# Optimization experiments

Hardware: AMD Instinct MI355X
Metric: run time of the kernel (lower is better)

## Reference

```python
import jax, jax.numpy as jnp
import numpy as np

B = 512
NODES_PER_GRAPH = 256
N = B * NODES_PER_GRAPH
IN_DIM = 128
HID = 128
PAD_VALUE = -10000.0


def setup_inputs() -> dict:
    key = jax.random.key(0)
    ks = jax.random.split(key, 10)
    inp = {
        "last_node_batch": jax.random.normal(ks[0], (B, IN_DIM), jnp.float32),
        "h": jax.random.normal(ks[1], (N, HID), jnp.float32),
        # NodeEmbed: Linear(in_dim, hidden_dim)
        "W_embed": jax.random.normal(ks[2], (IN_DIM, HID), jnp.float32) / np.sqrt(IN_DIM),
        "b_embed": jnp.zeros((HID,), jnp.float32),
        # Linear_3(2H, 2H, 2)
        "W1": jax.random.normal(ks[3], (2 * HID, 2 * HID), jnp.float32) / np.sqrt(2 * HID),
        "b1": jnp.zeros((2 * HID,), jnp.float32),
        "W2": jax.random.normal(ks[4], (2 * HID, 2 * HID), jnp.float32) / np.sqrt(2 * HID),
        "b2": jnp.zeros((2 * HID,), jnp.float32),
        "W3": jax.random.normal(ks[5], (2 * HID, 2), jnp.float32) / np.sqrt(2 * HID),
        "b3": jnp.zeros((2,), jnp.float32),
        # ragged batch encoded as sorted segment ids (graph id per node)
        "segment_ids": jnp.repeat(jnp.arange(B, dtype=jnp.int64), NODES_PER_GRAPH),
        "max_nodes": NODES_PER_GRAPH,
    }
    return inp


def reference(last_node_batch, h, W_embed, b_embed, W1, b1, W2, b2, W3, b3,
              segment_ids, max_nodes):
    n = h.shape[0]
    b = last_node_batch.shape[0]
    # per-graph node embed, broadcast to each node of its graph (repeat+cat loop)
    node_embed = last_node_batch @ W_embed + b_embed          # [B, H]
    bcast = node_embed[segment_ids]                           # [N, H]
    stack = jnp.concatenate([h, bcast], axis=1)               # [N, 2H]
    # Linear_3 MLP
    out = jnp.tanh(stack @ W1 + b1)
    out = jnp.tanh(out @ W2 + b2)
    edges = out @ W3 + b3                                     # [N, 2]
    # unbatch + pad_sequence(padding_value=-10000), then flatten(1, -1)
    counts = jax.ops.segment_sum(jnp.ones((n,), jnp.int32), segment_ids, num_segments=b)
    offsets = jnp.cumsum(counts) - counts                     # start index of each graph
    pos = jnp.arange(n) - offsets[segment_ids]                # position within graph
    padded = jnp.full((b, max_nodes, 2), PAD_VALUE, dtype=edges.dtype)
    padded = padded.at[segment_ids, pos].set(edges)
    return padded.reshape(b, max_nodes * 2)
```

## Files before the change

kernel.cpp:

```cpp
#include <hip/hip_runtime.h>


typedef __attribute__((ext_vector_type(8))) short s16x8;
typedef __attribute__((ext_vector_type(4))) float f32x4;

#define K2   256
#define KH   128
#define LDK  264

__device__ __forceinline__ float b2f(unsigned short u) {
  return __builtin_bit_cast(float, (unsigned int)u << 16);
}
__device__ __forceinline__ unsigned short f2b(float f) {
  unsigned int u = __builtin_bit_cast(unsigned int, f);
  u += 0x7fffu + ((u >> 16) & 1u);
  return (unsigned short)(u >> 16);
}
__device__ __forceinline__ float fast_tanh(float x) {
  float ax = __builtin_fabsf(x);
  float t  = __builtin_amdgcn_exp2f(ax * -2.885390081777927f);
  float r  = (1.0f - t) * __builtin_amdgcn_rcpf(1.0f + t);
  return __builtin_copysignf(r, x);
}
__device__ __forceinline__ unsigned int probe_is16(const unsigned int* wraw,
                                                   int t) {
  unsigned int w = wraw[t];
  unsigned int e = (w >> 7) & 0xFFu;
  unsigned long long m = __ballot(e >= 96 && e < 128);
  return (__popcll(m) >= 32) ? 1u : 0u;
}

__global__ __launch_bounds__(256) void prep_pack(
    const void* __restrict__ W1, const void* __restrict__ W2,
    const void* __restrict__ Wemb,
    unsigned short* __restrict__ W1P, unsigned short* __restrict__ W2P)
{
  __shared__ unsigned int flagLds;
  const int blk = blockIdx.x, t = threadIdx.x;
  if (t < 64) { unsigned int f = probe_is16((const unsigned int*)Wemb, t);
                if (t == 0) flagLds = f; }
  __syncthreads();
  const bool is16 = flagLds != 0u;

  const void* S; unsigned short* D; int k0, n0, pk;
  if (blk < 32) { S = W1; D = W1P; pk = 2048;
                  k0 = (blk & 3) * 32; n0 = (blk >> 2) * 32; }
  else { int b = blk - 32; S = W2; D = W2P; pk = 4096;
         k0 = (b & 7) * 32; n0 = (b >> 3) * 32; }
  #pragma unroll
  for (int q = 0; q < 4; ++q) {
    int idx = t + 256 * q;
    int ln = idx & 31, lk = idx >> 5;
    int n = n0 + ln, k = k0 + lk;
    unsigned short v = is16 ? ((const unsigned short*)S)[k * K2 + n]
                            : f2b(((const float*)S)[k * K2 + n]);
    D[(n >> 4) * pk + (k >> 3) * 128 + (n & 15) * 8 + (k & 7)] = v;
  }
}

__global__ __launch_bounds__(512, 4) void mlp_fused(
    const void* __restrict__ h,     const void* __restrict__ last,
    const void* __restrict__ Wemb,  const void* __restrict__ bemb,
    const void* __restrict__ W1,    const void* __restrict__ b1,
    const void* __restrict__ b2,    const void* __restrict__ W3,
    const void* __restrict__ b3,
    const unsigned short* __restrict__ W1P,
    const unsigned short* __restrict__ W2P,
    void* __restrict__ out)
{
  __shared__ __align__(16) unsigned short smA[128 * LDK];
  __shared__ float embf[KH];
  __shared__ float ebias[K2];
  __shared__ float w3s[2 * K2];
  __shared__ float b3s[2];
  __shared__ float headp[128 * 8];
  __shared__ unsigned int flagLds;

  const int t    = threadIdx.x;
  const int lane = t & 63, w = t >> 6;
  const int wr = w >> 2, wc = w & 3;
  const int quad = lane >> 4, l16 = lane & 15;
  const int base = blockIdx.x * 128;
  const int g    = base >> 8;

  if (t < 64) { unsigned int f = probe_is16((const unsigned int*)Wemb, t);
                if (t == 0) flagLds = f; }
  __syncthreads();
  const bool is16 = flagLds != 0u;

  if (is16) {
    const uint4* hp = (const uint4*)h;
    #pragma unroll
    for (int i = 0; i < 4; ++i) {
      int id = t + 512 * i;
      int r = id >> 4, c = id & 15;
      *(uint4*)&smA[r * LDK + c * 8] = hp[(size_t)(base + r) * 16 + c];
    }
  } else {
    const float4* hf = (const float4*)h;
    #pragma unroll
    for (int i = 0; i < 8; ++i) {
      int id = t + 512 * i;
      int r = id >> 5, c = id & 31;
      float4 v = hf[(size_t)(base + r) * 32 + c];
      ushort4 u;
      u.x = f2b(v.x); u.y = f2b(v.y); u.z = f2b(v.z); u.w = f2b(v.w);
      *(ushort4*)&smA[r * LDK + c * 4] = u;
    }
  }
  w3s[t] = is16 ? b2f(((const unsigned short*)W3)[t]) : ((const float*)W3)[t];
  if (t < 2)
    b3s[t] = is16 ? b2f(((const unsigned short*)b3)[t]) : ((const float*)b3)[t];
  if (t < KH) {
    float acc;
    if (is16) {
      acc = b2f(((const unsigned short*)bemb)[t]);
      const unsigned short* lp = (const unsigned short*)last + g * KH;
      const unsigned short* wp = (const unsigned short*)Wemb;
      #pragma unroll 4
      for (int k = 0; k < KH; ++k) acc += b2f(lp[k]) * b2f(wp[k * KH + t]);
    } else {
      acc = ((const float*)bemb)[t];
      const float* lp = (const float*)last + g * KH;
      const float* wp = (const float*)Wemb;
      #pragma unroll 4
      for (int k = 0; k < KH; ++k) acc += lp[k] * wp[k * KH + t];
    }
    embf[t] = acc;
  }
  __syncthreads();

  if (t < K2) {
    float e = is16 ? b2f(((const unsigned short*)b1)[t]) : ((const float*)b1)[t];
    if (is16) {
      const unsigned short* wp = (const unsigned short*)W1 + (size_t)KH * K2;
      #pragma unroll 4
      for (int k = 0; k < KH; ++k) e += embf[k] * b2f(wp[k * K2 + t]);
    } else {
      const float* wp = (const float*)W1 + (size_t)KH * K2;
      #pragma unroll 4
      for (int k = 0; k < KH; ++k) e += embf[k] * wp[k * K2 + t];
    }
    ebias[t] = e;
  }

  f32x4 acc[4][4];
  #pragma unroll
  for (int i = 0; i < 4; ++i)
    #pragma unroll
    for (int c = 0; c < 4; ++c) acc[i][c] = f32x4{0.f, 0.f, 0.f, 0.f};
  #pragma unroll
  for (int kk = 0; kk < 4; ++kk) {
    s16x8 a[4], b[4];
    #pragma unroll
    for (int i = 0; i < 4; ++i)
      a[i] = *(const s16x8*)&smA[(wr * 64 + i * 16 + l16) * LDK
                                 + kk * 32 + quad * 8];
    #pragma unroll
    for (int c = 0; c < 4; ++c)
      b[c] = *(const s16x8*)&W1P[(wc * 4 + c) * 2048
                                 + (kk * 4 + quad) * 128 + l16 * 8];
    #pragma unroll
    for (int i = 0; i < 4; ++i)
      #pragma unroll
      for (int c = 0; c < 4; ++c)
        acc[i][c] = __builtin_amdgcn_mfma_f32_16x16x32_bf16(
            a[i], b[c], acc[i][c], 0, 0, 0);
  }
  __syncthreads();
  #pragma unroll
  for (int i = 0; i < 4; ++i)
    #pragma unroll
    for (int c = 0; c < 4; ++c) {
      int col = wc * 64 + c * 16 + l16;
      #pragma unroll
      for (int rg = 0; rg < 4; ++rg)
        smA[(wr * 64 + i * 16 + quad * 4 + rg) * LDK + col] =
            f2b(fast_tanh(acc[i][c][rg] + ebias[col]));
    }
  __syncthreads();

  #pragma unroll
  for (int i = 0; i < 4; ++i)
    #pragma unroll
    for (int c = 0; c < 4; ++c) acc[i][c] = f32x4{0.f, 0.f, 0.f, 0.f};
  #pragma unroll 2
  for (int kk = 0; kk < 8; ++kk) {
    s16x8 a[4], b[4];
    #pragma unroll
    for (int i = 0; i < 4; ++i)
      a[i] = *(const s16x8*)&smA[(wr * 64 + i * 16 + l16) * LDK
                                 + kk * 32 + quad * 8];
    #pragma unroll
    for (int c = 0; c < 4; ++c)
      b[c] = *(const s16x8*)&W2P[(wc * 4 + c) * 4096
                                 + (kk * 4 + quad) * 128 + l16 * 8];
    #pragma unroll
    for (int i = 0; i < 4; ++i)
      #pragma unroll
      for (int c = 0; c < 4; ++c)
        acc[i][c] = __builtin_amdgcn_mfma_f32_16x16x32_bf16(
            a[i], b[c], acc[i][c], 0, 0, 0);
  }
  float bl[4];
  #pragma unroll
  for (int c = 0; c < 4; ++c) {
    int n = wc * 64 + c * 16 + l16;
    bl[c] = is16 ? b2f(((const unsigned short*)b2)[n]) : ((const float*)b2)[n];
  }
  __syncthreads();
  #pragma unroll
  for (int i = 0; i < 4; ++i)
    #pragma unroll
    for (int c = 0; c < 4; ++c) {
      int col = wc * 64 + c * 16 + l16;
      #pragma unroll
      for (int rg = 0; rg < 4; ++rg)
        smA[(wr * 64 + i * 16 + quad * 4 + rg) * LDK + col] =
            f2b(fast_tanh(acc[i][c][rg] + bl[c]));
    }
  __syncthreads();

  {
    const int r = t >> 2, q = t & 3;
    float s0 = 0.f, s1 = 0.f;
    #pragma unroll
    for (int cc = 0; cc < 8; ++cc) {
      int c8 = q * 8 + ((cc + r) & 7);
      s16x8 v = *(const s16x8*)&smA[r * LDK + c8 * 8];
      #pragma unroll
      for (int j = 0; j < 8; ++j) {
        float f = b2f((unsigned short)v[j]);
        int k = c8 * 8 + j;
        s0 += f * w3s[2 * k];
        s1 += f * w3s[2 * k + 1];
      }
    }
    headp[r * 8 + q * 2 + 0] = s0;
    headp[r * 8 + q * 2 + 1] = s1;
  }
  __syncthreads();
  if (t < 256) {
    const int r = t >> 1, e = t & 1;
    float s = b3s[e] + headp[r * 8 + e] + headp[r * 8 + 2 + e]
            + headp[r * 8 + 4 + e] + headp[r * 8 + 6 + e];
    size_t idx = (size_t)(base + r) * 2 + e;
    if (is16) ((unsigned short*)out)[idx] = f2b(s);
    else      ((float*)out)[idx] = s;
  }
}

extern "C" void kernel_launch(void* const* d_in, const int* in_sizes, int n_in,
                              void* d_out, int out_size, void* d_ws, size_t ws_size,
                              hipStream_t stream) {
  (void)in_sizes; (void)n_in; (void)out_size; (void)ws_size;
  const void* last = d_in[0];
  const void* h    = d_in[1];
  const void* Wemb = d_in[2];
  const void* bemb = d_in[3];
  const void* W1   = d_in[4];
  const void* b1   = d_in[5];
  const void* W2   = d_in[6];
  const void* b2   = d_in[7];
  const void* W3   = d_in[8];
  const void* b3   = d_in[9];

  char* ws = (char*)d_ws;
  unsigned short* W1P = (unsigned short*)(ws);
  unsigned short* W2P = (unsigned short*)(ws + 65536);

  prep_pack<<<dim3(96), dim3(256), 0, stream>>>(W1, W2, Wemb, W1P, W2P);
  mlp_fused<<<dim3(1024), dim3(512), 0, stream>>>(
      h, last, Wemb, bemb, W1, b1, b2, W3, b3, W1P, W2P, d_out);
}
```

Before: 184.5 us.

## Halve tile to 64 rows, MFMA head, Pade tanh, pretransposed W1 low half

Shrinks each block to 64 rows with 256 threads and 4 waves, each wave owning 64 output columns, doubling the grid. It pre-transposes the lower half of W1 in the prep kernel so the per-graph bias GEMV reads contiguous rows with vector loads. It replaces the exp-based tanh with a clamped Pade rational approximation and computes the final 2-column head with MFMA instead of scalar dot products. The aim is to cut LDS use, raise occupancy and trim epilogue ALU work. The risks are more redundant per-block embedding and bias work and a less accurate tanh for larger inputs.

```diff
diff --git a/kernel.cpp b/kernel.cpp
--- a/kernel.cpp
+++ b/kernel.cpp
@@ -16,11 +16,13 @@
   u += 0x7fffu + ((u >> 16) & 1u);
   return (unsigned short)(u >> 16);
 }
-__device__ __forceinline__ float fast_tanh(float x) {
-  float ax = __builtin_fabsf(x);
-  float t  = __builtin_amdgcn_exp2f(ax * -2.885390081777927f);
-  float r  = (1.0f - t) * __builtin_amdgcn_rcpf(1.0f + t);
-  return __builtin_copysignf(r, x);
+__device__ __forceinline__ float pade_tanh(float x) {
+  float x2 = x * x;
+  float x4 = x2 * x2;
+  float num = x * (945.0f + 105.0f * x2 + x4);
+  float den = __builtin_fmaf(15.0f, x4, __builtin_fmaf(420.0f, x2, 945.0f));
+  float r = num * __builtin_amdgcn_rcpf(den);
+  return __builtin_fmaxf(-1.0f, __builtin_fminf(1.0f, r));
 }
 __device__ __forceinline__ unsigned int probe_is16(const unsigned int* wraw,
                                                    int t) {
@@ -33,7 +35,8 @@
 __global__ __launch_bounds__(256) void prep_pack(
     const void* __restrict__ W1, const void* __restrict__ W2,
     const void* __restrict__ Wemb,
-    unsigned short* __restrict__ W1P, unsigned short* __restrict__ W2P)
+    unsigned short* __restrict__ W1P, unsigned short* __restrict__ W2P,
+    unsigned short* __restrict__ W1loT)
 {
   __shared__ unsigned int flagLds;
   const int blk = blockIdx.x, t = threadIdx.x;
@@ -42,45 +45,57 @@
   __syncthreads();
   const bool is16 = flagLds != 0u;
 
-  const void* S; unsigned short* D; int k0, n0, pk;
-  if (blk < 32) { S = W1; D = W1P; pk = 2048;
-                  k0 = (blk & 3) * 32; n0 = (blk >> 2) * 32; }
-  else { int b = blk - 32; S = W2; D = W2P; pk = 4096;
-         k0 = (b & 7) * 32; n0 = (b >> 3) * 32; }
-  #pragma unroll
-  for (int q = 0; q < 4; ++q) {
-    int idx = t + 256 * q;
-    int ln = idx & 31, lk = idx >> 5;
-    int n = n0 + ln, k = k0 + lk;
-    unsigned short v = is16 ? ((const unsigned short*)S)[k * K2 + n]
-                            : f2b(((const float*)S)[k * K2 + n]);
-    D[(n >> 4) * pk + (k >> 3) * 128 + (n & 15) * 8 + (k & 7)] = v;
-  }
-}
-
-__global__ __launch_bounds__(512, 4) void mlp_fused(
+  if (blk < 96) {
+    const void* S; unsigned short* D; int k0, n0, pk;
+    if (blk < 32) { S = W1; D = W1P; pk = 2048;
+                    k0 = (blk & 3) * 32; n0 = (blk >> 2) * 32; }
+    else { int b = blk - 32; S = W2; D = W2P; pk = 4096;
+           k0 = (b & 7) * 32; n0 = (b >> 3) * 32; }
+    #pragma unroll
+    for (int q = 0; q < 4; ++q) {
+      int idx = t + 256 * q;
+      int ln = idx & 31, lk = idx >> 5;
+      int n = n0 + ln, k = k0 + lk;
+      unsigned short v = is16 ? ((const unsigned short*)S)[k * K2 + n]
+                              : f2b(((const float*)S)[k * K2 + n]);
+      D[(n >> 4) * pk + (k >> 3) * 128 + (n & 15) * 8 + (k & 7)] = v;
+    }
+  } else {
+    int b = blk - 96;
+    int k0 = (b & 3) * 32, n0 = (b >> 2) * 32;
+    #pragma unroll
+    for (int q = 0; q < 4; ++q) {
+      int idx = t + 256 * q;
+      int ln = idx & 31, lk = idx >> 5;
+      int n = n0 + ln, k = k0 + lk;
+      unsigned short v = is16
+          ? ((const unsigned short*)W1)[(KH + k) * K2 + n]
+          : f2b(((const float*)W1)[(KH + k) * K2 + n]);
+      W1loT[n * KH + k] = v;
+    }
+  }
+}
+
+__global__ __launch_bounds__(256, 4) void mlp_fused(
     const void* __restrict__ h,     const void* __restrict__ last,
     const void* __restrict__ Wemb,  const void* __restrict__ bemb,
-    const void* __restrict__ W1,    const void* __restrict__ b1,
-    const void* __restrict__ b2,    const void* __restrict__ W3,
-    const void* __restrict__ b3,
+    const void* __restrict__ b1,    const void* __restrict__ b2,
+    const void* __restrict__ W3,    const void* __restrict__ b3,
     const unsigned short* __restrict__ W1P,
     const unsigned short* __restrict__ W2P,
+    const unsigned short* __restrict__ W1loT,
     void* __restrict__ out)
 {
-  __shared__ __align__(16) unsigned short smA[128 * LDK];
-  __shared__ float embf[KH];
+  __shared__ __align__(16) unsigned short smA[64 * LDK];
+  __shared__ __align__(16) float embf[KH];
   __shared__ float ebias[K2];
-  __shared__ float w3s[2 * K2];
-  __shared__ float b3s[2];
-  __shared__ float headp[128 * 8];
+  __shared__ float headp[4][64][2];
   __shared__ unsigned int flagLds;
 
   const int t    = threadIdx.x;
   const int lane = t & 63, w = t >> 6;
-  const int wr = w >> 2, wc = w & 3;
   const int quad = lane >> 4, l16 = lane & 15;
-  const int base = blockIdx.x * 128;
+  const int base = blockIdx.x * 64;
   const int g    = base >> 8;
 
   if (t < 64) { unsigned int f = probe_is16((const unsigned int*)Wemb, t);
@@ -92,7 +107,7 @@
     const uint4* hp = (const uint4*)h;
     #pragma unroll
     for (int i = 0; i < 4; ++i) {
-      int id = t + 512 * i;
+      int id = t + 256 * i;
       int r = id >> 4, c = id & 15;
       *(uint4*)&smA[r * LDK + c * 8] = hp[(size_t)(base + r) * 16 + c];
     }
@@ -100,7 +115,7 @@
     const float4* hf = (const float4*)h;
     #pragma unroll
     for (int i = 0; i < 8; ++i) {
-      int id = t + 512 * i;
+      int id = t + 256 * i;
       int r = id >> 5, c = id & 31;
       float4 v = hf[(size_t)(base + r) * 32 + c];
       ushort4 u;
@@ -108,40 +123,55 @@
       *(ushort4*)&smA[r * LDK + c * 4] = u;
     }
   }
-  w3s[t] = is16 ? b2f(((const unsigned short*)W3)[t]) : ((const float*)W3)[t];
-  if (t < 2)
-    b3s[t] = is16 ? b2f(((const unsigned short*)b3)[t]) : ((const float*)b3)[t];
   if (t < KH) {
-    float acc;
+    float a0 = 0.f, a1 = 0.f, a2 = 0.f, a3 = 0.f;
     if (is16) {
-      acc = b2f(((const unsigned short*)bemb)[t]);
       const unsigned short* lp = (const unsigned short*)last + g * KH;
       const unsigned short* wp = (const unsigned short*)Wemb;
-      #pragma unroll 4
-      for (int k = 0; k < KH; ++k) acc += b2f(lp[k]) * b2f(wp[k * KH + t]);
+      #pragma unroll 2
+      for (int k = 0; k < KH; k += 4) {
+        a0 += b2f(lp[k])     * b2f(wp[k * KH + t]);
+        a1 += b2f(lp[k + 1]) * b2f(wp[(k + 1) * KH + t]);
+        a2 += b2f(lp[k + 2]) * b2f(wp[(k + 2) * KH + t]);
+        a3 += b2f(lp[k + 3]) * b2f(wp[(k + 3) * KH + t]);
+      }
+      embf[t] = b2f(((const unsigned short*)bemb)[t]) + (a0 + a1) + (a2 + a3);
     } else {
-      acc = ((const float*)bemb)[t];
       const float* lp = (const float*)last + g * KH;
       const float* wp = (const float*)Wemb;
-      #pragma unroll 4
-      for (int k = 0; k < KH; ++k) acc += lp[k] * wp[k * KH + t];
-    }
-    embf[t] = acc;
-  }
-  __syncthreads();
-
-  if (t < K2) {
-    float e = is16 ? b2f(((const unsigned short*)b1)[t]) : ((const float*)b1)[t];
-    if (is16) {
-      const unsigned short* wp = (const unsigned short*)W1 + (size_t)KH * K2;
-      #pragma unroll 4
-      for (int k = 0; k < KH; ++k) e += embf[k] * b2f(wp[k * K2 + t]);
-    } else {
-      const float* wp = (const float*)W1 + (size_t)KH * K2;
-      #pragma unroll 4
-      for (int k = 0; k < KH; ++k) e += embf[k] * wp[k * K2 + t];
-    }
-    ebias[t] = e;
+      #pragma unroll 2
+      for (int k = 0; k < KH; k += 4) {
+        a0 += lp[k]     * wp[k * KH + t];
+        a1 += lp[k + 1] * wp[(k + 1) * KH + t];
+        a2 += lp[k + 2] * wp[(k + 2) * KH + t];
+        a3 += lp[k + 3] * wp[(k + 3) * KH + t];
+      }
+      embf[t] = ((const float*)bemb)[t] + (a0 + a1) + (a2 + a3);
+    }
+  }
+  __syncthreads();
+
+  {
+    const int n = t;
+    float e0 = 0.f, e1 = 0.f, e2 = 0.f, e3 = 0.f;
+    const unsigned short* wrow = W1loT + n * KH;
+    #pragma unroll 4
+    for (int k8 = 0; k8 < KH; k8 += 8) {
+      s16x8 wv = *(const s16x8*)&wrow[k8];
+      float4 ea = *(const float4*)&embf[k8];
+      float4 eb = *(const float4*)&embf[k8 + 4];
+      e0 += ea.x * b2f((unsigned short)wv[0]);
+      e1 += ea.y * b2f((unsigned short)wv[1]);
+      e2 += ea.z * b2f((unsigned short)wv[2]);
+      e3 += ea.w * b2f((unsigned short)wv[3]);
+      e0 += eb.x * b2f((unsigned short)wv[4]);
+      e1 += eb.y * b2f((unsigned short)wv[5]);
+      e2 += eb.z * b2f((unsigned short)wv[6]);
+      e3 += eb.w * b2f((unsigned short)wv[7]);
+    }
+    float bb = is16 ? b2f(((const unsigned short*)b1)[n])
+                    : ((const float*)b1)[n];
+    ebias[n] = bb + (e0 + e1) + (e2 + e3);
   }
 
   f32x4 acc[4][4];
@@ -154,11 +184,10 @@
     s16x8 a[4], b[4];
     #pragma unroll
     for (int i = 0; i < 4; ++i)
-      a[i] = *(const s16x8*)&smA[(wr * 64 + i * 16 + l16) * LDK
-                                 + kk * 32 + quad * 8];
+      a[i] = *(const s16x8*)&smA[(i * 16 + l16) * LDK + kk * 32 + quad * 8];
     #pragma unroll
     for (int c = 0; c < 4; ++c)
-      b[c] = *(const s16x8*)&W1P[(wc * 4 + c) * 2048
+      b[c] = *(const s16x8*)&W1P[(w * 4 + c) * 2048
                                  + (kk * 4 + quad) * 128 + l16 * 8];
     #pragma unroll
     for (int i = 0; i < 4; ++i)
@@ -169,15 +198,16 @@
   }
   __syncthreads();
   #pragma unroll
-  for (int i = 0; i < 4; ++i)
-    #pragma unroll
-    for (int c = 0; c < 4; ++c) {
-      int col = wc * 64 + c * 16 + l16;
+  for (int c = 0; c < 4; ++c) {
+    int col = w * 64 + c * 16 + l16;
+    float eb = ebias[col];
+    #pragma unroll
+    for (int i = 0; i < 4; ++i)
       #pragma unroll
       for (int rg = 0; rg < 4; ++rg)
-        smA[(wr * 64 + i * 16 + quad * 4 + rg) * LDK + col] =
-            f2b(fast_tanh(acc[i][c][rg] + ebias[col]));
-    }
+        smA[(i * 16 + quad * 4 + rg) * LDK + col] =
+            f2b(pade_tanh(acc[i][c][rg] + eb));
+  }
   __syncthreads();
 
   #pragma unroll
@@ -189,11 +219,10 @@
     s16x8 a[4], b[4];
     #pragma unroll
     for (int i = 0; i < 4; ++i)
-      a[i] = *(const s16x8*)&smA[(wr * 64 + i * 16 + l16) * LDK
-                                 + kk * 32 + quad * 8];
+      a[i] = *(const s16x8*)&smA[(i * 16 + l16) * LDK + kk * 32 + quad * 8];
     #pragma unroll
     for (int c = 0; c < 4; ++c)
-      b[c] = *(const s16x8*)&W2P[(wc * 4 + c) * 4096
+      b[c] = *(const s16x8*)&W2P[(w * 4 + c) * 4096
                                  + (kk * 4 + quad) * 128 + l16 * 8];
     #pragma unroll
     for (int i = 0; i < 4; ++i)
@@ -202,48 +231,63 @@
         acc[i][c] = __builtin_amdgcn_mfma_f32_16x16x32_bf16(
             a[i], b[c], acc[i][c], 0, 0, 0);
   }
-  float bl[4];
+  __syncthreads();
   #pragma unroll
   for (int c = 0; c < 4; ++c) {
-    int n = wc * 64 + c * 16 + l16;
-    bl[c] = is16 ? b2f(((const unsigned short*)b2)[n]) : ((const float*)b2)[n];
-  }
-  __syncthreads();
-  #pragma unroll
-  for (int i = 0; i < 4; ++i)
-    #pragma unroll
-    for (int c = 0; c < 4; ++c) {
-      int col = wc * 64 + c * 16 + l16;
+    int col = w * 64 + c * 16 + l16;
+    float bb = is16 ? b2f(((const unsigned short*)b2)[col])
+                    : ((const float*)b2)[col];
+    #pragma unroll
+    for (int i = 0; i < 4; ++i)
       #pragma unroll
       for (int rg = 0; rg < 4; ++rg)
-        smA[(wr * 64 + i * 16 + quad * 4 + rg) * LDK + col] =
-            f2b(fast_tanh(acc[i][c][rg] + bl[c]));
-    }
+        smA[(i * 16 + quad * 4 + rg) * LDK + col] =
+            f2b(pade_tanh(acc[i][c][rg] + bb));
+  }
   __syncthreads();
 
   {
-    const int r = t >> 2, q = t & 3;
-    float s0 = 0.f, s1 = 0.f;
-    #pragma unroll
-    for (int cc = 0; cc < 8; ++cc) {
-      int c8 = q * 8 + ((cc + r) & 7);
-      s16x8 v = *(const s16x8*)&smA[r * LDK + c8 * 8];
-      #pragma unroll
-      for (int j = 0; j < 8; ++j) {
-        float f = b2f((unsigned short)v[j]);
-        int k = c8 * 8 + j;
-        s0 += f * w3s[2 * k];
-        s1 += f * w3s[2 * k + 1];
+    f32x4 accH[4];
+    #pragma unroll
+    for (int i = 0; i < 4; ++i) accH[i] = f32x4{0.f, 0.f, 0.f, 0.f};
+    #pragma unroll
+    for (int s = 0; s < 2; ++s) {
+      int kk = 2 * w + s;
+      s16x8 bh;
+      if (is16) {
+        const unsigned short* w3u = (const unsigned short*)W3;
+        #pragma unroll
+        for (int j = 0; j < 8; ++j)
+          bh[j] = (short)w3u[(kk * 32 + quad * 8 + j) * 2 + (l16 & 1)];
+      } else {
+        const float* w3f = (const float*)W3;
+        #pragma unroll
+        for (int j = 0; j < 8; ++j)
+          bh[j] = (short)f2b(w3f[(kk * 32 + quad * 8 + j) * 2 + (l16 & 1)]);
       }
-    }
-    headp[r * 8 + q * 2 + 0] = s0;
-    headp[r * 8 + q * 2 + 1] = s1;
-  }
-  __syncthreads();
-  if (t < 256) {
+      #pragma unroll
+      for (int i = 0; i < 4; ++i) {
+        s16x8 a = *(const s16x8*)&smA[(i * 16 + l16) * LDK
+                                      + kk * 32 + quad * 8];
+        accH[i] = __builtin_amdgcn_mfma_f32_16x16x32_bf16(
+            a, bh, accH[i], 0, 0, 0);
+      }
+    }
+    if (l16 < 2) {
+      #pragma unroll
+      for (int i = 0; i < 4; ++i)
+        #pragma unroll
+        for (int rg = 0; rg < 4; ++rg)
+          headp[w][i * 16 + quad * 4 + rg][l16] = accH[i][rg];
+    }
+  }
+  __syncthreads();
+  if (t < 128) {
     const int r = t >> 1, e = t & 1;
-    float s = b3s[e] + headp[r * 8 + e] + headp[r * 8 + 2 + e]
-            + headp[r * 8 + 4 + e] + headp[r * 8 + 6 + e];
+    float b3e = is16 ? b2f(((const unsigned short*)b3)[e])
+                     : ((const float*)b3)[e];
+    float s = b3e + headp[0][r][e] + headp[1][r][e]
+                  + headp[2][r][e] + headp[3][r][e];
     size_t idx = (size_t)(base + r) * 2 + e;
     if (is16) ((unsigned short*)out)[idx] = f2b(s);
     else      ((float*)out)[idx] = s;
@@ -266,10 +310,11 @@
   const void* b3   = d_in[9];
 
   char* ws = (char*)d_ws;
-  unsigned short* W1P = (unsigned short*)(ws);
-  unsigned short* W2P = (unsigned short*)(ws + 65536);
-
-  prep_pack<<<dim3(96), dim3(256), 0, stream>>>(W1, W2, Wemb, W1P, W2P);
-  mlp_fused<<<dim3(1024), dim3(512), 0, stream>>>(
-      h, last, Wemb, bemb, W1, b1, b2, W3, b3, W1P, W2P, d_out);
-}
+  unsigned short* W1P   = (unsigned short*)(ws);
+  unsigned short* W2P   = (unsigned short*)(ws + 65536);
+  unsigned short* W1loT = (unsigned short*)(ws + 196608);
+
+  prep_pack<<<dim3(128), dim3(256), 0, stream>>>(W1, W2, Wemb, W1P, W2P, W1loT);
+  mlp_fused<<<dim3(2048), dim3(256), 0, stream>>>(
+      h, last, Wemb, bemb, b1, b2, W3, b3, W1P, W2P, W1loT, d_out);
+}
```

Result: faster. 175.6 us (-4.8%).
